# Performance work log

Hardware: AMD Instinct MI355X
Metric: run time of the kernel (lower is better)

## Reference

```python
import jax, jax.numpy as jnp
import numpy as np

EPS = 1e-5  # torch BatchNorm2d default


def _conv1x1(x, w):
    # x: [n, cin, h, w], w: [cout, cin] (1x1 conv == per-pixel matmul)
    return jnp.einsum('nchw,oc->nohw', x, w)


def _bn(x, gamma, beta, mean, var):
    # inference-mode BatchNorm2d over channel dim
    scale = gamma * jax.lax.rsqrt(var + EPS)
    shift = beta - mean * scale
    return x * scale[None, :, None, None] + shift[None, :, None, None]


def setup_inputs() -> dict:
    key = jax.random.key(0)
    ks = jax.random.split(key, 24)
    n, c, h, w = 16, 256, 64, 64
    width, planes = c // 2, c
    inp = {
        'x': jax.random.normal(ks[0], (n, c, h, w), jnp.float32),
        'w_theta': jax.random.normal(ks[1], (width, c), jnp.float32) * 0.05,
        'w_phi': jax.random.normal(ks[2], (width, c), jnp.float32) * 0.05,
        'w_g': jax.random.normal(ks[3], (width, c), jnp.float32) * 0.05,
        'w_zeta': jax.random.normal(ks[4], (planes, width), jnp.float32) * 0.05,
    }
    for i, (name, dim) in enumerate([('bn1', width), ('bn2', width), ('bn3', width), ('bn4', planes)]):
        k = 5 + 4 * i
        inp[f'{name}_gamma'] = jax.random.uniform(ks[k], (dim,), jnp.float32, 0.5, 1.5)
        inp[f'{name}_beta'] = jax.random.normal(ks[k + 1], (dim,), jnp.float32) * 0.1
        inp[f'{name}_mean'] = jax.random.normal(ks[k + 2], (dim,), jnp.float32) * 0.1
        inp[f'{name}_var'] = jax.random.uniform(ks[k + 3], (dim,), jnp.float32, 0.5, 1.5)
    return inp


def reference(x, w_theta, w_phi, w_g, w_zeta,
              bn1_gamma, bn1_beta, bn1_mean, bn1_var,
              bn2_gamma, bn2_beta, bn2_mean, bn2_var,
              bn3_gamma, bn3_beta, bn3_mean, bn3_var,
              bn4_gamma, bn4_beta, bn4_mean, bn4_var):
    n, c, h, w = x.shape
    theta = jax.nn.relu(_bn(_conv1x1(x, w_theta), bn1_gamma, bn1_beta, bn1_mean, bn1_var))
    phi = jax.nn.relu(_bn(_conv1x1(x, w_phi), bn2_gamma, bn2_beta, bn2_mean, bn2_var))
    g = jax.nn.relu(_bn(_conv1x1(x, w_g), bn3_gamma, bn3_beta, bn3_mean, bn3_var))

    width = theta.shape[1]
    hw = h * w
    theta = theta.reshape(n, width, hw)  # [n, C', S]
    phi = phi.reshape(n, width, hw)      # [n, C', S]
    g = g.reshape(n, width, hw)          # [n, C', S]

    # (theta^T @ phi) @ g^T == theta^T @ (phi @ g^T): no softmax, so associativity
    # lets us contract over pixels first -> O(S*C'^2) instead of O(S^2*C').
    kv = jnp.einsum('ncs,nds->ncd', phi, g)      # [n, C', C']
    out = jnp.einsum('ncs,ncd->nsd', theta, kv)  # [n, S, C']

    # faithful to torch: reshape (not transpose) [n, S, C'] -> [n, C', h, w]
    out = out.reshape(n, width, h, w)
    out = _bn(_conv1x1(out, w_zeta), bn4_gamma, bn4_beta, bn4_mean, bn4_var)
    return jax.nn.relu(out + x)
```

## Files before the change

kernel.cpp:

```cpp
#include <hip/hip_runtime.h>

#define BN_EPS 1e-5f

typedef unsigned short u16;
typedef __bf16 bf16x8 __attribute__((ext_vector_type(8)));
typedef float floatx4 __attribute__((ext_vector_type(4)));
typedef u16 u16x8 __attribute__((ext_vector_type(8)));

__device__ __forceinline__ u16 f2bf(float f) {
    union { float f; unsigned int u; } v; v.f = f;
    unsigned int r = (v.u + 0x7fffu + ((v.u >> 16) & 1u)) >> 16;
    return (u16)r;
}

__device__ __forceinline__ void gld16(const void* gsrc, void* ldst) {
    __builtin_amdgcn_global_load_lds(
        (const __attribute__((address_space(1))) unsigned int*)gsrc,
        (__attribute__((address_space(3))) unsigned int*)ldst, 16, 0, 0);
}

__device__ __forceinline__ int addsw(int seg, int s) {
    return (seg + (s & 7) + ((s >> 3) & 7)) & 7;
}

__global__ __launch_bounds__(256) void prep_kernel(
    const float* __restrict__ wt, const float* __restrict__ wp,
    const float* __restrict__ wg, const float* __restrict__ wz,
    const float* __restrict__ g1, const float* __restrict__ b1,
    const float* __restrict__ m1, const float* __restrict__ v1,
    const float* __restrict__ g2, const float* __restrict__ b2,
    const float* __restrict__ m2, const float* __restrict__ v2,
    const float* __restrict__ g3, const float* __restrict__ b3,
    const float* __restrict__ m3, const float* __restrict__ v3,
    const float* __restrict__ g4, const float* __restrict__ b4,
    const float* __restrict__ m4, const float* __restrict__ v4,
    u16* __restrict__ W1bf, float* __restrict__ shift1,
    u16* __restrict__ Wzbf, float* __restrict__ shift4)
{
    int id = blockIdx.x * 256 + threadIdx.x;
    if (id < 384 * 256) {
        int r = id >> 8, c = id & 255;
        int grp = r >> 7, ch = r & 127;
        const float* wsrc = grp == 0 ? wt : (grp == 1 ? wp : wg);
        const float* gg = grp == 0 ? g1 : (grp == 1 ? g2 : g3);
        const float* bb = grp == 0 ? b1 : (grp == 1 ? b2 : b3);
        const float* mm = grp == 0 ? m1 : (grp == 1 ? m2 : m3);
        const float* vv = grp == 0 ? v1 : (grp == 1 ? v2 : v3);
        float scale = gg[ch] * rsqrtf(vv[ch] + BN_EPS);
        W1bf[id] = f2bf(wsrc[ch * 256 + c] * scale);
        if (c == 0) shift1[r] = bb[ch] - mm[ch] * scale;
    }
    if (id < 256 * 128) {
        int o = id >> 7;
        float scale = g4[o] * rsqrtf(v4[o] + BN_EPS);
        Wzbf[id] = f2bf(wz[id] * scale);
        if ((id & 127) == 0) shift4[o] = b4[o] - m4[o] * scale;
    }
}

__global__ __launch_bounds__(256) void gemm1_kernel(
    const float* __restrict__ x, const u16* __restrict__ W1,
    const float* __restrict__ shift1, u16* __restrict__ tpg)
{
    const int st = blockIdx.x, mt = blockIdx.y, n = blockIdx.z;
    const int tid = threadIdx.x;
    const int w = tid >> 6, lane = tid & 63;
    const int quad = lane >> 4, l16 = lane & 15;

    __shared__ __align__(16) u16 ldsA[128 * 64];
    __shared__ __align__(16) u16 ldsB[128 * 64];

    floatx4 acc[2][8];
#pragma unroll
    for (int i = 0; i < 2; ++i)
#pragma unroll
        for (int j = 0; j < 8; ++j) acc[i][j] = floatx4{0.f, 0.f, 0.f, 0.f};

    const int s4 = tid & 31;
    const int cg = tid >> 5;
    const float* xbase = x + ((size_t)n * 256) * 4096 + st * 128;
    unsigned int* ldsBdw = (unsigned int*)ldsB;

    for (int kc = 0; kc < 4; ++kc) {
#pragma unroll
        for (int i = 0; i < 4; ++i) {
            int op = w * 4 + i;
            int r = op * 8 + (lane >> 3);
            int lseg = (lane & 7) ^ (r & 7);
            const u16* src = W1 + (size_t)(mt * 128 + r) * 256 + kc * 64 + lseg * 8;
            gld16(src, ldsA + op * 512);
        }
#pragma unroll
        for (int p = 0; p < 4; ++p) {
            int c0 = 2 * cg + 16 * p;
            const float4* r0 = (const float4*)(xbase + (size_t)(kc * 64 + c0) * 4096) + s4;
            const float4* r1 = (const float4*)(xbase + (size_t)(kc * 64 + c0 + 1) * 4096) + s4;
            float4 v0 = *r0, v1 = *r1;
            int cp = c0 >> 1, slog = cp >> 2, dwin = cp & 3;
#pragma unroll
            for (int j = 0; j < 4; ++j) {
                int s = 4 * s4 + j;
                unsigned int pk = (unsigned int)f2bf(((const float*)&v0)[j])
                                | ((unsigned int)f2bf(((const float*)&v1)[j]) << 16);
                ldsBdw[s * 32 + addsw(slog, s) * 4 + dwin] = pk;
            }
        }
        __syncthreads();

#pragma unroll
        for (int kk = 0; kk < 2; ++kk) {
            bf16x8 a[2];
#pragma unroll
            for (int mi = 0; mi < 2; ++mi) {
                int r = w * 32 + mi * 16 + l16;
                int phys = (kk * 4 + quad) ^ (r & 7);
                a[mi] = *(const bf16x8*)(ldsA + r * 64 + phys * 8);
            }
#pragma unroll
            for (int ni = 0; ni < 8; ++ni) {
                int s = ni * 16 + l16;
                int phys = addsw(kk * 4 + quad, s);
                bf16x8 b = *(const bf16x8*)(ldsB + s * 64 + phys * 8);
#pragma unroll
                for (int mi = 0; mi < 2; ++mi)
                    acc[mi][ni] = __builtin_amdgcn_mfma_f32_16x16x32_bf16(
                        a[mi], b, acc[mi][ni], 0, 0, 0);
            }
        }
        __syncthreads();
    }

#pragma unroll
    for (int mi = 0; mi < 2; ++mi)
#pragma unroll
        for (int r = 0; r < 4; ++r) {
            int oc = mt * 128 + w * 32 + mi * 16 + quad * 4 + r;
            float sh = shift1[oc];
#pragma unroll
            for (int ni = 0; ni < 8; ++ni) {
                int s = st * 128 + ni * 16 + l16;
                float val = acc[mi][ni][r] + sh;
                val = val > 0.f ? val : 0.f;
                tpg[((size_t)n * 384 + oc) * 4096 + s] = f2bf(val);
            }
        }
}

__global__ __launch_bounds__(256) void gemm2_kernel(
    const u16* __restrict__ tpg, float* __restrict__ partials)
{
    const int kc = blockIdx.x, n = blockIdx.y;
    const int tid = threadIdx.x;
    const int wave = tid >> 6, lane = tid & 63;
    const int quad = lane >> 4, l16 = lane & 15;

    floatx4 acc[2][8];
#pragma unroll
    for (int i = 0; i < 2; ++i)
#pragma unroll
        for (int j = 0; j < 8; ++j) acc[i][j] = floatx4{0.f, 0.f, 0.f, 0.f};

    const u16* gbase = tpg + ((size_t)n * 384 + 256) * 4096;
    const u16* pbase = tpg + ((size_t)n * 384 + 128) * 4096;

#pragma unroll
    for (int kk = 0; kk < 8; ++kk) {
        int sb = kc * 256 + kk * 32 + quad * 8;
        bf16x8 a[2];
#pragma unroll
        for (int mi = 0; mi < 2; ++mi) {
            int d = wave * 32 + mi * 16 + l16;
            a[mi] = *reinterpret_cast<const bf16x8*>(gbase + (size_t)d * 4096 + sb);
        }
#pragma unroll
        for (int ci = 0; ci < 8; ++ci) {
            int cc = ci * 16 + l16;
            bf16x8 b = *reinterpret_cast<const bf16x8*>(pbase + (size_t)cc * 4096 + sb);
#pragma unroll
            for (int mi = 0; mi < 2; ++mi)
                acc[mi][ci] = __builtin_amdgcn_mfma_f32_16x16x32_bf16(
                    a[mi], b, acc[mi][ci], 0, 0, 0);
        }
    }

    float* outp = partials + (size_t)(n * 16 + kc) * 16384;
#pragma unroll
    for (int mi = 0; mi < 2; ++mi)
#pragma unroll
        for (int r = 0; r < 4; ++r) {
            int d = wave * 32 + mi * 16 + quad * 4 + r;
#pragma unroll
            for (int ci = 0; ci < 8; ++ci)
                outp[d * 128 + ci * 16 + l16] = acc[mi][ci][r];
        }
}

__global__ __launch_bounds__(256) void kv_reduce_kernel(
    const float* __restrict__ partials, u16* __restrict__ kvT)
{
    int n = blockIdx.y;
    int idx = blockIdx.x * 256 + threadIdx.x;
    float s = 0.f;
#pragma unroll
    for (int kc = 0; kc < 16; ++kc)
        s += partials[(size_t)(n * 16 + kc) * 16384 + idx];
    kvT[(size_t)n * 16384 + idx] = f2bf(s);
}

__global__ __launch_bounds__(256) void gemm3_kernel(
    const u16* __restrict__ tpg, const u16* __restrict__ kvT,
    u16* __restrict__ out_sd)
{
    const int st = blockIdx.x, n = blockIdx.y;
    const int tid = threadIdx.x;
    const int w = tid >> 6, lane = tid & 63;
    const int quad = lane >> 4, l16 = lane & 15;

    __shared__ __align__(16) u16 ldsT[128 * 64];
    __shared__ __align__(16) u16 ldsK[128 * 64];

    floatx4 acc[2][8];
#pragma unroll
    for (int i = 0; i < 2; ++i)
#pragma unroll
        for (int j = 0; j < 8; ++j) acc[i][j] = floatx4{0.f, 0.f, 0.f, 0.f};

    const int sl = tid & 15;
    const int cg = tid >> 4;
    const u16* tbase = tpg + (size_t)n * 384 * 4096 + st * 128;
    const u16* kbase = kvT + (size_t)n * 16384;
    unsigned int* ldsTdw = (unsigned int*)ldsT;

    for (int kc = 0; kc < 2; ++kc) {
#pragma unroll
        for (int i = 0; i < 4; ++i) {
            int op = w * 4 + i;
            int r = op * 8 + (lane >> 3);
            int lseg = (lane & 7) ^ (r & 7);
            gld16(kbase + (size_t)r * 128 + kc * 64 + lseg * 8, ldsK + op * 512);
        }
#pragma unroll
        for (int p = 0; p < 2; ++p) {
            int c0 = 2 * cg + 32 * p;
            u16x8 t0 = *(const u16x8*)(tbase + (size_t)(kc * 64 + c0) * 4096 + 8 * sl);
            u16x8 t1 = *(const u16x8*)(tbase + (size_t)(kc * 64 + c0 + 1) * 4096 + 8 * sl);
            int cp = c0 >> 1, slog = cp >> 2, dwin = cp & 3;
#pragma unroll
            for (int j = 0; j < 8; ++j) {
                int s = 8 * sl + j;
                unsigned int pk = (unsigned int)t0[j] | ((unsigned int)t1[j] << 16);
                ldsTdw[s * 32 + addsw(slog, s) * 4 + dwin] = pk;
            }
        }
        __syncthreads();

#pragma unroll
        for (int kk = 0; kk < 2; ++kk) {
            bf16x8 a[2];
#pragma unroll
            for (int mi = 0; mi < 2; ++mi) {
                int s = w * 32 + mi * 16 + l16;
                int phys = addsw(kk * 4 + quad, s);
                a[mi] = *(const bf16x8*)(ldsT + s * 64 + phys * 8);
            }
#pragma unroll
            for (int di = 0; di < 8; ++di) {
                int d = di * 16 + l16;
                int phys = (kk * 4 + quad) ^ (d & 7);
                bf16x8 b = *(const bf16x8*)(ldsK + d * 64 + phys * 8);
#pragma unroll
                for (int mi = 0; mi < 2; ++mi)
                    acc[mi][di] = __builtin_amdgcn_mfma_f32_16x16x32_bf16(
                        a[mi], b, acc[mi][di], 0, 0, 0);
            }
        }
        __syncthreads();
    }

#pragma unroll
    for (int mi = 0; mi < 2; ++mi)
#pragma unroll
        for (int r = 0; r < 4; ++r) {
            int s = st * 128 + w * 32 + mi * 16 + quad * 4 + r;
#pragma unroll
            for (int di = 0; di < 8; ++di)
                out_sd[(size_t)n * 524288 + (size_t)s * 128 + di * 16 + l16] =
                    f2bf(acc[mi][di][r]);
        }
}

__global__ __launch_bounds__(256) void gemm4_kernel(
    const u16* __restrict__ out_sd, const u16* __restrict__ Wz,
    const float* __restrict__ shift4, const float* __restrict__ x,
    float* __restrict__ out)
{
    const int st = blockIdx.x, ot = blockIdx.y, n = blockIdx.z;
    const int tid = threadIdx.x;
    const int w = tid >> 6, lane = tid & 63;
    const int quad = lane >> 4, l16 = lane & 15;

    __shared__ __align__(16) u16 ldsY[128 * 64];
    __shared__ __align__(16) u16 ldsW[128 * 64];

    floatx4 acc[2][8];
#pragma unroll
    for (int i = 0; i < 2; ++i)
#pragma unroll
        for (int j = 0; j < 8; ++j) acc[i][j] = floatx4{0.f, 0.f, 0.f, 0.f};

    const int sl = tid & 15;
    const int cg = tid >> 4;
    const u16* ybase = out_sd + (size_t)n * 524288 + st * 128;
    unsigned int* ldsYdw = (unsigned int*)ldsY;

    for (int kc = 0; kc < 2; ++kc) {
#pragma unroll
        for (int i = 0; i < 4; ++i) {
            int op = w * 4 + i;
            int r = op * 8 + (lane >> 3);
            int lseg = (lane & 7) ^ (r & 7);
            gld16(Wz + (size_t)(ot * 128 + r) * 128 + kc * 64 + lseg * 8, ldsW + op * 512);
        }
#pragma unroll
        for (int p = 0; p < 2; ++p) {
            int c0 = 2 * cg + 32 * p;
            u16x8 t0 = *(const u16x8*)(ybase + (size_t)(kc * 64 + c0) * 4096 + 8 * sl);
            u16x8 t1 = *(const u16x8*)(ybase + (size_t)(kc * 64 + c0 + 1) * 4096 + 8 * sl);
            int cp = c0 >> 1, slog = cp >> 2, dwin = cp & 3;
#pragma unroll
            for (int j = 0; j < 8; ++j) {
                int s = 8 * sl + j;
                unsigned int pk = (unsigned int)t0[j] | ((unsigned int)t1[j] << 16);
                ldsYdw[s * 32 + addsw(slog, s) * 4 + dwin] = pk;
            }
        }
        __syncthreads();

#pragma unroll
        for (int kk = 0; kk < 2; ++kk) {
            bf16x8 a[2];
#pragma unroll
            for (int mi = 0; mi < 2; ++mi) {
                int r = w * 32 + mi * 16 + l16;
                int phys = (kk * 4 + quad) ^ (r & 7);
                a[mi] = *(const bf16x8*)(ldsW + r * 64 + phys * 8);
            }
#pragma unroll
            for (int ni = 0; ni < 8; ++ni) {
                int s = ni * 16 + l16;
                int phys = addsw(kk * 4 + quad, s);
                bf16x8 b = *(const bf16x8*)(ldsY + s * 64 + phys * 8);
#pragma unroll
                for (int mi = 0; mi < 2; ++mi)
                    acc[mi][ni] = __builtin_amdgcn_mfma_f32_16x16x32_bf16(
                        a[mi], b, acc[mi][ni], 0, 0, 0);
            }
        }
        __syncthreads();
    }

#pragma unroll
    for (int mi = 0; mi < 2; ++mi)
#pragma unroll
        for (int r = 0; r < 4; ++r) {
            int o = ot * 128 + w * 32 + mi * 16 + quad * 4 + r;
            float sh = shift4[o];
#pragma unroll
            for (int ni = 0; ni < 8; ++ni) {
                int s2 = st * 128 + ni * 16 + l16;
                size_t idx = ((size_t)n * 256 + o) * 4096 + s2;
                float val = acc[mi][ni][r] + sh + x[idx];
                out[idx] = val > 0.f ? val : 0.f;
            }
        }
}

extern "C" void kernel_launch(void* const* d_in, const int* in_sizes, int n_in,
                              void* d_out, int out_size, void* d_ws, size_t ws_size,
                              hipStream_t stream)
{
    const float* x  = (const float*)d_in[0];
    const float* wt = (const float*)d_in[1];
    const float* wp = (const float*)d_in[2];
    const float* wg = (const float*)d_in[3];
    const float* wz = (const float*)d_in[4];
    const float* bn[16];
    for (int i = 0; i < 16; ++i) bn[i] = (const float*)d_in[5 + i];

    char* ws = (char*)d_ws;
    u16*   W1bf     = (u16*)  (ws + 0);
    float* shift1   = (float*)(ws + 196608);
    u16*   Wzbf     = (u16*)  (ws + 198144);
    float* shift4   = (float*)(ws + 263680);
    u16*   tpg      = (u16*)  (ws + 264704);
    float* partials = (float*)(ws + 50596352);
    u16*   kvT      = (u16*)  (ws + 67373568);
    u16*   out_sd   = (u16*)  (ws + 67897856);
    float* out = (float*)d_out;

    prep_kernel<<<384, 256, 0, stream>>>(
        wt, wp, wg, wz,
        bn[0], bn[1], bn[2], bn[3],
        bn[4], bn[5], bn[6], bn[7],
        bn[8], bn[9], bn[10], bn[11],
        bn[12], bn[13], bn[14], bn[15],
        W1bf, shift1, Wzbf, shift4);

    gemm1_kernel<<<dim3(32, 3, 16), 256, 0, stream>>>(x, W1bf, shift1, tpg);
    gemm2_kernel<<<dim3(16, 16), 256, 0, stream>>>(tpg, partials);
    kv_reduce_kernel<<<dim3(64, 16), 256, 0, stream>>>(partials, kvT);
    gemm3_kernel<<<dim3(32, 16), 256, 0, stream>>>(tpg, kvT, out_sd);
    gemm4_kernel<<<dim3(32, 2, 16), 256, 0, stream>>>(out_sd, Wzbf, shift4, x, out);
}
```

Measured before the change: 228.6 us.

## Store theta pixel-major, stage gemm2 through LDS, prefetch inputs in gemm1/gemm4

gemm1 now writes theta transposed ([s][c]) as packed 4-wide bf16 stores, so gemm3 can load it with direct global-to-LDS copies instead of a register transpose. phi/g go to a separate buffer. gemm2 moves to 512 threads and stages phi/g tiles through swizzled LDS instead of reading strided global memory per lane. The kv reduction is vectorised to float4, and gemm1 and gemm4 prefetch the next K chunk of activations into registers during the current iteration. These changes add register pressure and a new workspace layout.

```diff
diff --git a/kernel.cpp b/kernel.cpp
--- a/kernel.cpp
+++ b/kernel.cpp
@@ -5,6 +5,7 @@
 typedef unsigned short u16;
 typedef __bf16 bf16x8 __attribute__((ext_vector_type(8)));
 typedef float floatx4 __attribute__((ext_vector_type(4)));
+typedef u16 u16x4 __attribute__((ext_vector_type(4)));
 typedef u16 u16x8 __attribute__((ext_vector_type(8)));
 
 __device__ __forceinline__ u16 f2bf(float f) {
@@ -60,7 +61,8 @@
 
 __global__ __launch_bounds__(256) void gemm1_kernel(
     const float* __restrict__ x, const u16* __restrict__ W1,
-    const float* __restrict__ shift1, u16* __restrict__ tpg)
+    const float* __restrict__ shift1,
+    u16* __restrict__ theta_sm, u16* __restrict__ pg)
 {
     const int st = blockIdx.x, mt = blockIdx.y, n = blockIdx.z;
     const int tid = threadIdx.x;
@@ -81,28 +83,40 @@
     const float* xbase = x + ((size_t)n * 256) * 4096 + st * 128;
     unsigned int* ldsBdw = (unsigned int*)ldsB;
 
+    float4 xv0[4], xv1[4];
+#pragma unroll
+    for (int p = 0; p < 4; ++p) {
+        int c0 = 2 * cg + 16 * p;
+        xv0[p] = *((const float4*)(xbase + (size_t)c0 * 4096) + s4);
+        xv1[p] = *((const float4*)(xbase + (size_t)(c0 + 1) * 4096) + s4);
+    }
+
     for (int kc = 0; kc < 4; ++kc) {
+#pragma unroll
+        for (int p = 0; p < 4; ++p) {
+            int cp = cg + 8 * p, slog = cp >> 2, dwin = cp & 3;
+#pragma unroll
+            for (int j = 0; j < 4; ++j) {
+                int s = 4 * s4 + j;
+                unsigned int pk = (unsigned int)f2bf(((const float*)&xv0[p])[j])
+                                | ((unsigned int)f2bf(((const float*)&xv1[p])[j]) << 16);
+                ldsBdw[s * 32 + addsw(slog, s) * 4 + dwin] = pk;
+            }
+        }
 #pragma unroll
         for (int i = 0; i < 4; ++i) {
             int op = w * 4 + i;
             int r = op * 8 + (lane >> 3);
             int lseg = (lane & 7) ^ (r & 7);
-            const u16* src = W1 + (size_t)(mt * 128 + r) * 256 + kc * 64 + lseg * 8;
-            gld16(src, ldsA + op * 512);
-        }
-#pragma unroll
-        for (int p = 0; p < 4; ++p) {
-            int c0 = 2 * cg + 16 * p;
-            const float4* r0 = (const float4*)(xbase + (size_t)(kc * 64 + c0) * 4096) + s4;
-            const float4* r1 = (const float4*)(xbase + (size_t)(kc * 64 + c0 + 1) * 4096) + s4;
-            float4 v0 = *r0, v1 = *r1;
-            int cp = c0 >> 1, slog = cp >> 2, dwin = cp & 3;
-#pragma unroll
-            for (int j = 0; j < 4; ++j) {
-                int s = 4 * s4 + j;
-                unsigned int pk = (unsigned int)f2bf(((const float*)&v0)[j])
-                                | ((unsigned int)f2bf(((const float*)&v1)[j]) << 16);
-                ldsBdw[s * 32 + addsw(slog, s) * 4 + dwin] = pk;
+            gld16(W1 + (size_t)(mt * 128 + r) * 256 + kc * 64 + lseg * 8,
+                  ldsA + op * 512);
+        }
+        if (kc < 3) {
+#pragma unroll
+            for (int p = 0; p < 4; ++p) {
+                int c0 = 2 * cg + 16 * p;
+                xv0[p] = *((const float4*)(xbase + (size_t)((kc + 1) * 64 + c0) * 4096) + s4);
+                xv1[p] = *((const float4*)(xbase + (size_t)((kc + 1) * 64 + c0 + 1) * 4096) + s4);
             }
         }
         __syncthreads();
@@ -130,57 +144,97 @@
         __syncthreads();
     }
 
-#pragma unroll
-    for (int mi = 0; mi < 2; ++mi)
-#pragma unroll
-        for (int r = 0; r < 4; ++r) {
-            int oc = mt * 128 + w * 32 + mi * 16 + quad * 4 + r;
-            float sh = shift1[oc];
+    if (mt == 0) {
+#pragma unroll
+        for (int mi = 0; mi < 2; ++mi) {
+            int ocb = w * 32 + mi * 16 + quad * 4;
+            float sh0 = shift1[ocb + 0], sh1 = shift1[ocb + 1];
+            float sh2 = shift1[ocb + 2], sh3 = shift1[ocb + 3];
 #pragma unroll
             for (int ni = 0; ni < 8; ++ni) {
                 int s = st * 128 + ni * 16 + l16;
-                float val = acc[mi][ni][r] + sh;
-                val = val > 0.f ? val : 0.f;
-                tpg[((size_t)n * 384 + oc) * 4096 + s] = f2bf(val);
-            }
-        }
-}
-
-__global__ __launch_bounds__(256) void gemm2_kernel(
-    const u16* __restrict__ tpg, float* __restrict__ partials)
+                float v0 = acc[mi][ni][0] + sh0, v1 = acc[mi][ni][1] + sh1;
+                float v2 = acc[mi][ni][2] + sh2, v3 = acc[mi][ni][3] + sh3;
+                u16x4 pk;
+                pk[0] = f2bf(v0 > 0.f ? v0 : 0.f);
+                pk[1] = f2bf(v1 > 0.f ? v1 : 0.f);
+                pk[2] = f2bf(v2 > 0.f ? v2 : 0.f);
+                pk[3] = f2bf(v3 > 0.f ? v3 : 0.f);
+                *(u16x4*)(theta_sm + (size_t)n * 524288 + (size_t)s * 128 + ocb) = pk;
+            }
+        }
+    } else {
+#pragma unroll
+        for (int mi = 0; mi < 2; ++mi)
+#pragma unroll
+            for (int r = 0; r < 4; ++r) {
+                int oc = mt * 128 + w * 32 + mi * 16 + quad * 4 + r;
+                int prow = (mt - 1) * 128 + w * 32 + mi * 16 + quad * 4 + r;
+                float sh = shift1[oc];
+#pragma unroll
+                for (int ni = 0; ni < 8; ++ni) {
+                    int s = st * 128 + ni * 16 + l16;
+                    float val = acc[mi][ni][r] + sh;
+                    val = val > 0.f ? val : 0.f;
+                    pg[(size_t)n * 1048576 + (size_t)prow * 4096 + s] = f2bf(val);
+                }
+            }
+    }
+}
+
+__global__ __launch_bounds__(512) void gemm2_kernel(
+    const u16* __restrict__ pg, float* __restrict__ partials)
 {
     const int kc = blockIdx.x, n = blockIdx.y;
     const int tid = threadIdx.x;
-    const int wave = tid >> 6, lane = tid & 63;
+    const int w = tid >> 6, lane = tid & 63;
     const int quad = lane >> 4, l16 = lane & 15;
 
-    floatx4 acc[2][8];
+    __shared__ __align__(16) u16 ldsG[128 * 64];
+    __shared__ __align__(16) u16 ldsP[128 * 64];
+
+    floatx4 acc[2][4];
 #pragma unroll
     for (int i = 0; i < 2; ++i)
 #pragma unroll
-        for (int j = 0; j < 8; ++j) acc[i][j] = floatx4{0.f, 0.f, 0.f, 0.f};
-
-    const u16* gbase = tpg + ((size_t)n * 384 + 256) * 4096;
-    const u16* pbase = tpg + ((size_t)n * 384 + 128) * 4096;
-
-#pragma unroll
-    for (int kk = 0; kk < 8; ++kk) {
-        int sb = kc * 256 + kk * 32 + quad * 8;
-        bf16x8 a[2];
-#pragma unroll
-        for (int mi = 0; mi < 2; ++mi) {
-            int d = wave * 32 + mi * 16 + l16;
-            a[mi] = *reinterpret_cast<const bf16x8*>(gbase + (size_t)d * 4096 + sb);
-        }
-#pragma unroll
-        for (int ci = 0; ci < 8; ++ci) {
-            int cc = ci * 16 + l16;
-            bf16x8 b = *reinterpret_cast<const bf16x8*>(pbase + (size_t)cc * 4096 + sb);
-#pragma unroll
-            for (int mi = 0; mi < 2; ++mi)
-                acc[mi][ci] = __builtin_amdgcn_mfma_f32_16x16x32_bf16(
-                    a[mi], b, acc[mi][ci], 0, 0, 0);
-        }
+        for (int j = 0; j < 4; ++j) acc[i][j] = floatx4{0.f, 0.f, 0.f, 0.f};
+
+    const int d0 = (w >> 1) * 32, c0 = (w & 1) * 64;
+    const u16* base = pg + (size_t)n * 1048576;
+
+    for (int ch = 0; ch < 4; ++ch) {
+        int s0 = kc * 256 + ch * 64;
+#pragma unroll
+        for (int i = 0; i < 2; ++i) {
+            int op = w * 2 + i;
+            int r = op * 8 + (lane >> 3);
+            int lseg = (lane & 7) ^ (r & 7);
+            gld16(base + (size_t)(128 + r) * 4096 + s0 + lseg * 8, ldsG + op * 512);
+            gld16(base + (size_t)r * 4096 + s0 + lseg * 8, ldsP + op * 512);
+        }
+        __syncthreads();
+
+#pragma unroll
+        for (int kk = 0; kk < 2; ++kk) {
+            bf16x8 a[2];
+#pragma unroll
+            for (int mi = 0; mi < 2; ++mi) {
+                int r = d0 + mi * 16 + l16;
+                int phys = (kk * 4 + quad) ^ (r & 7);
+                a[mi] = *(const bf16x8*)(ldsG + r * 64 + phys * 8);
+            }
+#pragma unroll
+            for (int ci = 0; ci < 4; ++ci) {
+                int r = c0 + ci * 16 + l16;
+                int phys = (kk * 4 + quad) ^ (r & 7);
+                bf16x8 b = *(const bf16x8*)(ldsP + r * 64 + phys * 8);
+#pragma unroll
+                for (int mi = 0; mi < 2; ++mi)
+                    acc[mi][ci] = __builtin_amdgcn_mfma_f32_16x16x32_bf16(
+                        a[mi], b, acc[mi][ci], 0, 0, 0);
+            }
+        }
+        __syncthreads();
     }
 
     float* outp = partials + (size_t)(n * 16 + kc) * 16384;
@@ -188,10 +242,10 @@
     for (int mi = 0; mi < 2; ++mi)
 #pragma unroll
         for (int r = 0; r < 4; ++r) {
-            int d = wave * 32 + mi * 16 + quad * 4 + r;
-#pragma unroll
-            for (int ci = 0; ci < 8; ++ci)
-                outp[d * 128 + ci * 16 + l16] = acc[mi][ci][r];
+            int d = d0 + mi * 16 + quad * 4 + r;
+#pragma unroll
+            for (int ci = 0; ci < 4; ++ci)
+                outp[d * 128 + c0 + ci * 16 + l16] = acc[mi][ci][r];
         }
 }
 
@@ -199,16 +253,20 @@
     const float* __restrict__ partials, u16* __restrict__ kvT)
 {
     int n = blockIdx.y;
-    int idx = blockIdx.x * 256 + threadIdx.x;
-    float s = 0.f;
-#pragma unroll
-    for (int kc = 0; kc < 16; ++kc)
-        s += partials[(size_t)(n * 16 + kc) * 16384 + idx];
-    kvT[(size_t)n * 16384 + idx] = f2bf(s);
+    int f4 = blockIdx.x * 256 + threadIdx.x;
+    const float4* p4 = (const float4*)partials;
+    float4 s = {0.f, 0.f, 0.f, 0.f};
+#pragma unroll
+    for (int kc = 0; kc < 16; ++kc) {
+        float4 v = p4[(size_t)(n * 16 + kc) * 4096 + f4];
+        s.x += v.x; s.y += v.y; s.z += v.z; s.w += v.w;
+    }
+    u16x4 o; o[0] = f2bf(s.x); o[1] = f2bf(s.y); o[2] = f2bf(s.z); o[3] = f2bf(s.w);
+    *(u16x4*)(kvT + (size_t)n * 16384 + f4 * 4) = o;
 }
 
 __global__ __launch_bounds__(256) void gemm3_kernel(
-    const u16* __restrict__ tpg, const u16* __restrict__ kvT,
+    const u16* __restrict__ theta_sm, const u16* __restrict__ kvT,
     u16* __restrict__ out_sd)
 {
     const int st = blockIdx.x, n = blockIdx.y;
@@ -225,32 +283,17 @@
 #pragma unroll
         for (int j = 0; j < 8; ++j) acc[i][j] = floatx4{0.f, 0.f, 0.f, 0.f};
 
-    const int sl = tid & 15;
-    const int cg = tid >> 4;
-    const u16* tbase = tpg + (size_t)n * 384 * 4096 + st * 128;
+    const u16* tbase = theta_sm + (size_t)n * 524288 + (size_t)st * 128 * 128;
     const u16* kbase = kvT + (size_t)n * 16384;
-    unsigned int* ldsTdw = (unsigned int*)ldsT;
-
-    for (int kc = 0; kc < 2; ++kc) {
+
+    for (int ch = 0; ch < 2; ++ch) {
 #pragma unroll
         for (int i = 0; i < 4; ++i) {
             int op = w * 4 + i;
             int r = op * 8 + (lane >> 3);
             int lseg = (lane & 7) ^ (r & 7);
-            gld16(kbase + (size_t)r * 128 + kc * 64 + lseg * 8, ldsK + op * 512);
-        }
-#pragma unroll
-        for (int p = 0; p < 2; ++p) {
-            int c0 = 2 * cg + 32 * p;
-            u16x8 t0 = *(const u16x8*)(tbase + (size_t)(kc * 64 + c0) * 4096 + 8 * sl);
-            u16x8 t1 = *(const u16x8*)(tbase + (size_t)(kc * 64 + c0 + 1) * 4096 + 8 * sl);
-            int cp = c0 >> 1, slog = cp >> 2, dwin = cp & 3;
-#pragma unroll
-            for (int j = 0; j < 8; ++j) {
-                int s = 8 * sl + j;
-                unsigned int pk = (unsigned int)t0[j] | ((unsigned int)t1[j] << 16);
-                ldsTdw[s * 32 + addsw(slog, s) * 4 + dwin] = pk;
-            }
+            gld16(tbase + (size_t)r * 128 + ch * 64 + lseg * 8, ldsT + op * 512);
+            gld16(kbase + (size_t)r * 128 + ch * 64 + lseg * 8, ldsK + op * 512);
         }
         __syncthreads();
 
@@ -259,15 +302,15 @@
             bf16x8 a[2];
 #pragma unroll
             for (int mi = 0; mi < 2; ++mi) {
-                int s = w * 32 + mi * 16 + l16;
-                int phys = addsw(kk * 4 + quad, s);
-                a[mi] = *(const bf16x8*)(ldsT + s * 64 + phys * 8);
+                int r = w * 32 + mi * 16 + l16;
+                int phys = (kk * 4 + quad) ^ (r & 7);
+                a[mi] = *(const bf16x8*)(ldsT + r * 64 + phys * 8);
             }
 #pragma unroll
             for (int di = 0; di < 8; ++di) {
-                int d = di * 16 + l16;
-                int phys = (kk * 4 + quad) ^ (d & 7);
-                bf16x8 b = *(const bf16x8*)(ldsK + d * 64 + phys * 8);
+                int r = di * 16 + l16;
+                int phys = (kk * 4 + quad) ^ (r & 7);
+                bf16x8 b = *(const bf16x8*)(ldsK + r * 64 + phys * 8);
 #pragma unroll
                 for (int mi = 0; mi < 2; ++mi)
                     acc[mi][di] = __builtin_amdgcn_mfma_f32_16x16x32_bf16(
@@ -313,7 +356,25 @@
     const u16* ybase = out_sd + (size_t)n * 524288 + st * 128;
     unsigned int* ldsYdw = (unsigned int*)ldsY;
 
+    u16x8 yv0[2], yv1[2];
+#pragma unroll
+    for (int p = 0; p < 2; ++p) {
+        int c0 = 2 * cg + 32 * p;
+        yv0[p] = *(const u16x8*)(ybase + (size_t)c0 * 4096 + 8 * sl);
+        yv1[p] = *(const u16x8*)(ybase + (size_t)(c0 + 1) * 4096 + 8 * sl);
+    }
+
     for (int kc = 0; kc < 2; ++kc) {
+#pragma unroll
+        for (int p = 0; p < 2; ++p) {
+            int cp = cg + 16 * p, slog = cp >> 2, dwin = cp & 3;
+#pragma unroll
+            for (int j = 0; j < 8; ++j) {
+                int s = 8 * sl + j;
+                unsigned int pk = (unsigned int)yv0[p][j] | ((unsigned int)yv1[p][j] << 16);
+                ldsYdw[s * 32 + addsw(slog, s) * 4 + dwin] = pk;
+            }
+        }
 #pragma unroll
         for (int i = 0; i < 4; ++i) {
             int op = w * 4 + i;
@@ -321,17 +382,12 @@
             int lseg = (lane & 7) ^ (r & 7);
             gld16(Wz + (size_t)(ot * 128 + r) * 128 + kc * 64 + lseg * 8, ldsW + op * 512);
         }
-#pragma unroll
-        for (int p = 0; p < 2; ++p) {
-            int c0 = 2 * cg + 32 * p;
-            u16x8 t0 = *(const u16x8*)(ybase + (size_t)(kc * 64 + c0) * 4096 + 8 * sl);
-            u16x8 t1 = *(const u16x8*)(ybase + (size_t)(kc * 64 + c0 + 1) * 4096 + 8 * sl);
-            int cp = c0 >> 1, slog = cp >> 2, dwin = cp & 3;
-#pragma unroll
-            for (int j = 0; j < 8; ++j) {
-                int s = 8 * sl + j;
-                unsigned int pk = (unsigned int)t0[j] | ((unsigned int)t1[j] << 16);
-                ldsYdw[s * 32 + addsw(slog, s) * 4 + dwin] = pk;
+        if (kc < 1) {
+#pragma unroll
+            for (int p = 0; p < 2; ++p) {
+                int c0 = 2 * cg + 32 * p;
+                yv0[p] = *(const u16x8*)(ybase + (size_t)(64 + c0) * 4096 + 8 * sl);
+                yv1[p] = *(const u16x8*)(ybase + (size_t)(64 + c0 + 1) * 4096 + 8 * sl);
             }
         }
         __syncthreads();
@@ -392,7 +448,8 @@
     float* shift1   = (float*)(ws + 196608);
     u16*   Wzbf     = (u16*)  (ws + 198144);
     float* shift4   = (float*)(ws + 263680);
-    u16*   tpg      = (u16*)  (ws + 264704);
+    u16*   theta_sm = (u16*)  (ws + 264704);
+    u16*   pg       = (u16*)  (ws + 17041920);
     float* partials = (float*)(ws + 50596352);
     u16*   kvT      = (u16*)  (ws + 67373568);
     u16*   out_sd   = (u16*)  (ws + 67897856);
@@ -406,9 +463,9 @@
         bn[12], bn[13], bn[14], bn[15],
         W1bf, shift1, Wzbf, shift4);
 
-    gemm1_kernel<<<dim3(32, 3, 16), 256, 0, stream>>>(x, W1bf, shift1, tpg);
-    gemm2_kernel<<<dim3(16, 16), 256, 0, stream>>>(tpg, partials);
-    kv_reduce_kernel<<<dim3(64, 16), 256, 0, stream>>>(partials, kvT);
-    gemm3_kernel<<<dim3(32, 16), 256, 0, stream>>>(tpg, kvT, out_sd);
+    gemm1_kernel<<<dim3(32, 3, 16), 256, 0, stream>>>(x, W1bf, shift1, theta_sm, pg);
+    gemm2_kernel<<<dim3(16, 16), 512, 0, stream>>>(pg, partials);
+    kv_reduce_kernel<<<dim3(16, 16), 256, 0, stream>>>(partials, kvT);
+    gemm3_kernel<<<dim3(32, 16), 256, 0, stream>>>(theta_sm, kvT, out_sd);
     gemm4_kernel<<<dim3(32, 2, 16), 256, 0, stream>>>(out_sd, Wzbf, shift4, x, out);
 }
```

New measurement: 219.8 us. 1.04x faster.
